# Kernel optimization log

Hardware: AMD Instinct MI355X
Metric: run time of the kernel (lower is better)

The kernel has to match this reference:

```python
import jax, jax.numpy as jnp
import numpy as np

N = 50000      # nodes
E = 800000     # edges (before self loops)
IN = 128       # in_channels
C = 64         # out_channels per head
H = 4          # heads (both layers)
NEG_SLOPE = 0.2


def setup_inputs():
    key = jax.random.key(0)
    ks = jax.random.split(key, 14)
    nrm = lambda k, sh, s: jax.random.normal(k, sh, dtype=jnp.float32) * s
    x = nrm(ks[0], (N, IN), 1.0)
    edge_index = jax.random.randint(ks[1], (2, E), 0, N, dtype=jnp.int32)
    batch = jnp.zeros((N,), dtype=jnp.int32)
    edge_attr = jax.random.uniform(ks[2], (E, 1), dtype=jnp.float32)
    # layer 1 params (PyG GATConv: lin, att_src, att_dst, lin_edge, att_edge, bias)
    W1 = nrm(ks[3], (IN, H * C), 1.0 / np.sqrt(IN))
    We1 = nrm(ks[4], (1, H * C), 1.0)
    att_s1 = nrm(ks[5], (H, C), 1.0 / np.sqrt(C))
    att_d1 = nrm(ks[6], (H, C), 1.0 / np.sqrt(C))
    att_e1 = nrm(ks[7], (H, C), 1.0 / np.sqrt(C))
    b1 = jnp.zeros((H * C,), dtype=jnp.float32)
    # layer 2 params (in = H*C = 256)
    W2 = nrm(ks[8], (H * C, H * C), 1.0 / np.sqrt(H * C))
    We2 = nrm(ks[9], (1, H * C), 1.0)
    att_s2 = nrm(ks[10], (H, C), 1.0 / np.sqrt(C))
    att_d2 = nrm(ks[11], (H, C), 1.0 / np.sqrt(C))
    att_e2 = nrm(ks[12], (H, C), 1.0 / np.sqrt(C))
    b2 = jnp.zeros((H * C,), dtype=jnp.float32)
    return dict(x=x, edge_index=edge_index, batch=batch, edge_attr=edge_attr,
                W1=W1, We1=We1, att_s1=att_s1, att_d1=att_d1, att_e1=att_e1, b1=b1,
                W2=W2, We2=We2, att_s2=att_s2, att_d2=att_d2, att_e2=att_e2, b2=b2)


def gat_layer(h_in, src, dst, e_attr, W, We, att_s, att_d, att_e, b):
    n = h_in.shape[0]
    h = (h_in @ W).reshape(n, H, C)                      # [N,H,C]
    a_src = jnp.einsum('nhc,hc->nh', h, att_s)           # [N,H]
    a_dst = jnp.einsum('nhc,hc->nh', h, att_d)
    e = (e_attr @ We).reshape(-1, H, C)                  # [E',H,C]
    a_edge = jnp.einsum('ehc,hc->eh', e, att_e)          # [E',H]
    alpha = jax.nn.leaky_relu(a_src[src] + a_dst[dst] + a_edge, NEG_SLOPE)
    # softmax over edges grouped by destination node
    amax = jax.ops.segment_max(alpha, dst, num_segments=n)
    amax = jnp.where(jnp.isfinite(amax), amax, 0.0)
    ex = jnp.exp(alpha - amax[dst])
    denom = jax.ops.segment_sum(ex, dst, num_segments=n)
    a = ex / (denom[dst] + 1e-16)                        # [E',H]
    out = jax.ops.segment_sum(a[:, :, None] * h[src], dst, num_segments=n)
    return out.reshape(n, H * C) + b


def reference(x, edge_index, batch, edge_attr,
              W1, We1, att_s1, att_d1, att_e1, b1,
              W2, We2, att_s2, att_d2, att_e2, b2):
    n = x.shape[0]
    # PyG GATConv default: add self loops, self-loop edge_attr = mean fill
    loop = jnp.arange(n, dtype=edge_index.dtype)
    src = jnp.concatenate([edge_index[0], loop])
    dst = jnp.concatenate([edge_index[1], loop])
    ea_fill = jnp.broadcast_to(edge_attr.mean(axis=0, keepdims=True), (n, edge_attr.shape[1]))
    ea = jnp.concatenate([edge_attr, ea_fill], axis=0)
    h1 = gat_layer(x, src, dst, ea, W1, We1, att_s1, att_d1, att_e1, b1)
    h2 = gat_layer(h1, src, dst, ea, W2, We2, att_s2, att_d2, att_e2, b2)
    return h2
```

## Files before the change

### kernel.cpp

```cpp
#include <hip/hip_runtime.h>

#define NEG_SLOPE 0.2f

typedef __attribute__((ext_vector_type(8))) short bf16x8;
typedef __attribute__((ext_vector_type(4))) float f32x4;

__device__ inline unsigned short f2bf(float x) {
  unsigned int u = __float_as_uint(x);
  u += 0x7fffu + ((u >> 16) & 1u);
  return (unsigned short)(u >> 16);
}

__device__ inline unsigned fkey(float x) {
  unsigned u = __float_as_uint(x);
  return (u >> 31) ? ~u : (u | 0x80000000u);
}
__device__ inline float fkey_dec(unsigned k) {
  unsigned u = (k & 0x80000000u) ? (k ^ 0x80000000u) : ~k;
  return __uint_as_float(u);
}


__global__ void hist_mean_kernel(const int* __restrict__ ei, const float* __restrict__ eattr,
                                 int* __restrict__ counts, float* __restrict__ part,
                                 int E, int Etot) {
  int e = blockIdx.x * blockDim.x + threadIdx.x;
  float s = 0.f;
  if (e < Etot) {
    int d = (e < E) ? ei[E + e] : (e - E);
    atomicAdd(&counts[d], 1);
    if (e < E) s = eattr[e];
  }
#pragma unroll
  for (int off = 1; off < 64; off <<= 1) s += __shfl_xor(s, off, 64);
  __shared__ float ws_[4];
  if ((threadIdx.x & 63) == 0) ws_[threadIdx.x >> 6] = s;
  __syncthreads();
  if (threadIdx.x == 0) part[blockIdx.x] = ws_[0] + ws_[1] + ws_[2] + ws_[3];
}

__global__ void scan_blocksum(const int* __restrict__ counts, int* __restrict__ bsum, int Nn) {
  int base = blockIdx.x * 4096 + threadIdx.x * 16;
  int s = 0;
#pragma unroll
  for (int i = 0; i < 16; i++) { int idx = base + i; if (idx < Nn) s += counts[idx]; }
#pragma unroll
  for (int off = 1; off < 64; off <<= 1) s += __shfl_xor(s, off, 64);
  __shared__ int ws_[4];
  if ((threadIdx.x & 63) == 0) ws_[threadIdx.x >> 6] = s;
  __syncthreads();
  if (threadIdx.x == 0) bsum[blockIdx.x] = ws_[0] + ws_[1] + ws_[2] + ws_[3];
}

__global__ void scan_offsets(int* bsum, int nb, int* rowptrN,
                             const float* __restrict__ meanpart, float* meanv,
                             int E, int npart) {
  int t = threadIdx.x;
  float f = 0.f;
  for (int i = t; i < npart; i += 64) f += meanpart[i];
#pragma unroll
  for (int off = 1; off < 64; off <<= 1) f += __shfl_xor(f, off, 64);
  if (t == 0) {
    *meanv = f / (float)E;
    int acc = 0;
    for (int i = 0; i < nb; i++) { int v = bsum[i]; bsum[i] = acc; acc += v; }
    *rowptrN = acc;
  }
}

__global__ void scan_final(const int* __restrict__ counts, const int* __restrict__ bsum,
                           int* __restrict__ rowptr, int* __restrict__ cursor, int Nn) {
  int base = blockIdx.x * 4096 + threadIdx.x * 16;
  int v[16]; int s = 0;
#pragma unroll
  for (int i = 0; i < 16; i++) { int idx = base + i; v[i] = (idx < Nn) ? counts[idx] : 0; s += v[i]; }
  int lane = threadIdx.x & 63, wv = threadIdx.x >> 6;
  int incl = s;
#pragma unroll
  for (int off = 1; off < 64; off <<= 1) {
    int y = __shfl_up(incl, off, 64);
    if (lane >= off) incl += y;
  }
  __shared__ int wtot[4];
  if (lane == 63) wtot[wv] = incl;
  __syncthreads();
  int run = bsum[blockIdx.x] + incl - s;
  for (int i = 0; i < wv; i++) run += wtot[i];
  for (int i = 0; i < 16; i++) {
    int idx = base + i;
    if (idx < Nn) { rowptr[idx] = run; cursor[idx] = run; }
    run += v[i];
  }
}

__global__ void scatter_kernel(const int* __restrict__ ei, const float* __restrict__ eattr,
                               const float* __restrict__ meanv,
                               int* __restrict__ cursor, int2* __restrict__ epack,
                               int E, int Etot) {
  int e = blockIdx.x * blockDim.x + threadIdx.x;
  if (e >= Etot) return;
  int d, s; float ea;
  if (e < E) { d = ei[E + e]; s = ei[e]; ea = eattr[e]; }
  else       { d = e - E;     s = e - E; ea = meanv[0]; }
  int pos = atomicAdd(&cursor[d], 1);
  epack[pos] = make_int2(s, __float_as_int(ea));
}

__global__ void wtrans_kernel(const float* __restrict__ W1, unsigned short* __restrict__ Wt1,
                              const float* __restrict__ W2, unsigned short* __restrict__ Wt2,
                              const float* __restrict__ We1, const float* __restrict__ atte1,
                              const float* __restrict__ We2, const float* __restrict__ atte2,
                              float* __restrict__ weatt1, float* __restrict__ weatt2) {
  int b = blockIdx.x;
  if (b >= 384) {
    int i = threadIdx.x;
#pragma unroll
    for (int l = 0; l < 2; l++) {
      const float* We = l ? We2 : We1;
      const float* at = l ? atte2 : atte1;
      float* wo = l ? weatt2 : weatt1;
      float p = We[i] * at[i];
#pragma unroll
      for (int off = 1; off < 64; off <<= 1) p += __shfl_xor(p, off, 64);
      if ((i & 63) == 0) wo[i >> 6] = p;
    }
    return;
  }
  const float* W; unsigned short* Wt; int K, t;
  if (b < 128) { W = W1; Wt = Wt1; K = 128; t = b * 256 + threadIdx.x; }
  else         { W = W2; Wt = Wt2; K = 256; t = (b - 128) * 256 + threadIdx.x; }
  int n = t & 255, k = t >> 8;
  if (k >= K) return;
  Wt[(size_t)n * K + k] = f2bf(W[(size_t)k * 256 + n]);
}


template <int AF32>
__device__ inline bf16x8 load_a_row(const void* Ain, int gr, int K, int kpos, int M) {
  bf16x8 v = {};
  if (gr < M) {
    if (AF32) {
      const float* src = (const float*)Ain + (size_t)gr * K + kpos;
      float4 f0 = *(const float4*)src;
      float4 f1 = *(const float4*)(src + 4);
      v[0] = (short)f2bf(f0.x); v[1] = (short)f2bf(f0.y);
      v[2] = (short)f2bf(f0.z); v[3] = (short)f2bf(f0.w);
      v[4] = (short)f2bf(f1.x); v[5] = (short)f2bf(f1.y);
      v[6] = (short)f2bf(f1.z); v[7] = (short)f2bf(f1.w);
    } else {
      v = *(const bf16x8*)((const unsigned short*)Ain + (size_t)gr * K + kpos);
    }
  }
  return v;
}

#define CS_STRIDE 264

template <int AF32>
__global__ __launch_bounds__(512) void gemm_att(const void* __restrict__ Ain,
                                                const unsigned short* __restrict__ Wt,
                                                unsigned short* __restrict__ Hb,
                                                const float* __restrict__ atts,
                                                const float* __restrict__ attd,
                                                float* __restrict__ asrc,
                                                float* __restrict__ adst,
                                                unsigned* __restrict__ gmaxk,
                                                int M, int K) {
  __shared__ __align__(16) short smem[(128 + 256) * 64];
  __shared__ float gmx[8];
  short* As = smem;
  short* Bs = smem + 128 * 64;
  short* Cs = smem;
  const int tid = threadIdx.x;
  const int lane = tid & 63, wv = tid >> 6;
  const int wm = wv >> 2, wn = wv & 3;
  const int l15 = lane & 15, l4 = lane >> 4;
  const int bm = blockIdx.x * 128;

  const int r0 = tid >> 3, kc = (tid & 7) * 8;
  const int nbB = tid >> 3, cB = (tid & 7) * 8;

  f32x4 acc[4][4] = {};
  bf16x8 ra0, ra1, rb0, rb1, rb2, rb3;

#define GLOAD_TILE(K0, A0, A1, B0, B1, B2, B3)                                 \
  {                                                                            \
    A0 = load_a_row<AF32>(Ain, bm + r0, K, (K0) + kc, M);                      \
    A1 = load_a_row<AF32>(Ain, bm + r0 + 64, K, (K0) + kc, M);                 \
    B0 = *(const bf16x8*)&Wt[(size_t)(nbB +   0) * K + (K0) + cB];             \
    B1 = *(const bf16x8*)&Wt[(size_t)(nbB +  64) * K + (K0) + cB];             \
    B2 = *(const bf16x8*)&Wt[(size_t)(nbB + 128) * K + (K0) + cB];             \
    B3 = *(const bf16x8*)&Wt[(size_t)(nbB + 192) * K + (K0) + cB];             \
  }

  GLOAD_TILE(0, ra0, ra1, rb0, rb1, rb2, rb3)

  for (int k0 = 0; k0 < K; k0 += 64) {
    *(bf16x8*)&As[((r0) * 64 + kc) ^ ((r0 & 7) << 3)] = ra0;
    *(bf16x8*)&As[((r0 + 64) * 64 + kc) ^ ((r0 & 7) << 3)] = ra1;
    *(bf16x8*)&Bs[((nbB) * 64 + cB) ^ ((nbB & 7) << 3)] = rb0;
    *(bf16x8*)&Bs[((nbB + 64) * 64 + cB) ^ ((nbB & 7) << 3)] = rb1;
    *(bf16x8*)&Bs[((nbB + 128) * 64 + cB) ^ ((nbB & 7) << 3)] = rb2;
    *(bf16x8*)&Bs[((nbB + 192) * 64 + cB) ^ ((nbB & 7) << 3)] = rb3;
    __syncthreads();

    bool more = (k0 + 64 < K);
    bf16x8 na0, na1, nb0, nb1, nb2, nb3;
    if (more) GLOAD_TILE(k0 + 64, na0, na1, nb0, nb1, nb2, nb3)

    bf16x8 af[4][2], bfr[4][2];
#pragma unroll
    for (int rt = 0; rt < 4; rt++)
#pragma unroll
      for (int ks = 0; ks < 2; ks++) {
        int row = wm * 64 + rt * 16 + l15;
        int kb = l4 * 8 + ks * 32;
        af[rt][ks] = *(const bf16x8*)&As[(row * 64 + kb) ^ ((row & 7) << 3)];
      }
#pragma unroll
    for (int ct = 0; ct < 4; ct++)
#pragma unroll
      for (int ks = 0; ks < 2; ks++) {
        int n = wn * 64 + ct * 16 + l15;
        int kb = l4 * 8 + ks * 32;
        bfr[ct][ks] = *(const bf16x8*)&Bs[(n * 64 + kb) ^ ((n & 7) << 3)];
      }
#pragma unroll
    for (int rt = 0; rt < 4; rt++)
#pragma unroll
      for (int ct = 0; ct < 4; ct++)
#pragma unroll
        for (int ks = 0; ks < 2; ks++)
          acc[rt][ct] = __builtin_amdgcn_mfma_f32_16x16x32_bf16(
              af[rt][ks], bfr[ct][ks], acc[rt][ct], 0, 0, 0);
    __syncthreads();

    if (more) { ra0 = na0; ra1 = na1; rb0 = nb0; rb1 = nb1; rb2 = nb2; rb3 = nb3; }
  }
#undef GLOAD_TILE

  float s_att[4], d_att[4];
#pragma unroll
  for (int ct = 0; ct < 4; ct++) {
    s_att[ct] = atts[wn * 64 + ct * 16 + l15];
    d_att[ct] = attd[wn * 64 + ct * 16 + l15];
  }
  float ps[4][4] = {}, pd[4][4] = {};
#pragma unroll
  for (int rt = 0; rt < 4; rt++)
#pragma unroll
    for (int ct = 0; ct < 4; ct++)
#pragma unroll
      for (int i = 0; i < 4; i++) {
        float v = acc[rt][ct][i];
        ps[rt][i] = fmaf(v, s_att[ct], ps[rt][i]);
        pd[rt][i] = fmaf(v, d_att[ct], pd[rt][i]);
      }

#pragma unroll
  for (int rt = 0; rt < 4; rt++)
#pragma unroll
    for (int i = 0; i < 4; i++) {
#pragma unroll
      for (int off = 1; off < 16; off <<= 1) {
        ps[rt][i] += __shfl_xor(ps[rt][i], off, 64);
        pd[rt][i] += __shfl_xor(pd[rt][i], off, 64);
      }
    }
  float mx = ps[0][0];
#pragma unroll
  for (int rt = 0; rt < 4; rt++)
#pragma unroll
    for (int i = 0; i < 4; i++) mx = fmaxf(mx, ps[rt][i]);
  mx = fmaxf(mx, __shfl_xor(mx, 16, 64));
  mx = fmaxf(mx, __shfl_xor(mx, 32, 64));
  if (lane == 0) gmx[wv] = mx;
  if (l15 == 0) {
#pragma unroll
    for (int rt = 0; rt < 4; rt++)
#pragma unroll
      for (int i = 0; i < 4; i++) {
        int gr = bm + wm * 64 + rt * 16 + l4 * 4 + i;
        if (gr < M) {
          asrc[gr * 4 + wn] = ps[rt][i];
          adst[gr * 4 + wn] = pd[rt][i];
        }
      }
  }

  for (int h = 0; h < 2; h++) {
    __syncthreads();
    if (wm == h) {
#pragma unroll
      for (int rt = 0; rt < 4; rt++)
#pragma unroll
        for (int ct = 0; ct < 4; ct++)
#pragma unroll
          for (int i = 0; i < 4; i++) {
            int lrow = rt * 16 + l4 * 4 + i;
            Cs[lrow * CS_STRIDE + wn * 64 + ct * 16 + l15] = f2bf(acc[rt][ct][i]);
          }
    }
    __syncthreads();
    int row = tid >> 3, seg = tid & 7;
    int gr = bm + h * 64 + row;
    if (gr < M) {
      const short* srcr = &Cs[row * CS_STRIDE + seg * 32];
      unsigned short* dstr = &Hb[(size_t)gr * 256 + seg * 32];
#pragma unroll
      for (int k = 0; k < 4; k++)
        *(uint4*)&dstr[k * 8] = *(const uint4*)&srcr[k * 8];
    }
  }

  if (wv < 4 && lane == 0) {
    float m2 = fmaxf(gmx[wv], gmx[wv + 4]);
    atomicMax(&gmaxk[wv * 32], fkey(m2));
  }
}


#define AGG_PH1(CNT)                                                        \
  int src = 0; float w = 0.f;                                               \
  if (il < (CNT)) {                                                         \
    int2 e = epack[p + il];                                                 \
    float al = fmaf(__int_as_float(e.y), wa, asrc[e.x * 4 + hh] + ad);      \
    al = fmaxf(al, NEG_SLOPE * al);                                         \
    w = __expf(al - b);                                                     \
    src = e.x;                                                              \
  }                                                                         \
  ssum += w;

#define AGG_GATHER(i)                                                       \
  {                                                                         \
    int sl = (i) | hb16;                                                    \
    int si = __shfl(src, sl, 64);                                           \
    float wi = __shfl(w, sl, 64);                                           \
    uint2 hv = *(const uint2*)&Hb[(size_t)((unsigned)si * 256u + co)];      \
    acc.x = fmaf(wi, __uint_as_float(hv.x << 16), acc.x);                   \
    acc.y = fmaf(wi, __uint_as_float(hv.x & 0xffff0000u), acc.y);           \
    acc.z = fmaf(wi, __uint_as_float(hv.y << 16), acc.z);                   \
    acc.w = fmaf(wi, __uint_as_float(hv.y & 0xffff0000u), acc.w);           \
  }

template <int OUTBF>
__global__ __launch_bounds__(256) void gat_agg(const unsigned short* __restrict__ Hb,
                                               const float* __restrict__ asrc,
                                               const float* __restrict__ adst,
                                               const int* __restrict__ rowptr,
                                               const int2* __restrict__ epack,
                                               const float* __restrict__ weatt,
                                               const unsigned* __restrict__ gmaxk,
                                               const float* __restrict__ bias,
                                               unsigned short* __restrict__ outb,
                                               float* __restrict__ outf, int Nn) {
  int wid = (blockIdx.x * blockDim.x + threadIdx.x) >> 6;
  int lane = threadIdx.x & 63;
  if (wid >= Nn) return;
  int beg = rowptr[wid], end = rowptr[wid + 1];
  int hh = lane >> 4;
  int il = lane & 15;
  int hb16 = lane & 48;
  float wa = weatt[hh];
  float ad = adst[wid * 4 + hh];
  float braw = ad + fkey_dec(gmaxk[hh * 32]) + fmaxf(wa, 0.f);
  float b = fmaxf(braw, NEG_SLOPE * braw);
  unsigned co = (unsigned)lane * 4u;

  float ssum = 0.f;
  float4 acc = {0.f, 0.f, 0.f, 0.f};

  int p = beg;
  for (; p + 16 <= end; p += 16) {
    AGG_PH1(16)
#pragma unroll
    for (int i = 0; i < 16; i++) AGG_GATHER(i)
  }
  int cnt = end - p;
  if (cnt > 0) {
    AGG_PH1(cnt)
    for (int i = 0; i < cnt; i++) AGG_GATHER(i)
  }

#pragma unroll
  for (int off = 1; off < 16; off <<= 1) ssum += __shfl_xor(ssum, off, 64);

  float inv = 1.f / (ssum + 1e-16f);
  float4 b4 = *(const float4*)&bias[co];
  float4 r;
  r.x = fmaf(acc.x, inv, b4.x);
  r.y = fmaf(acc.y, inv, b4.y);
  r.z = fmaf(acc.z, inv, b4.z);
  r.w = fmaf(acc.w, inv, b4.w);
  if (OUTBF) {
    unsigned lo = (unsigned)f2bf(r.x) | ((unsigned)f2bf(r.y) << 16);
    unsigned hi = (unsigned)f2bf(r.z) | ((unsigned)f2bf(r.w) << 16);
    *(uint2*)&outb[(size_t)wid * 256 + co] = make_uint2(lo, hi);
  } else {
    *(float4*)&outf[(size_t)wid * 256 + co] = r;
  }
}


extern "C" void kernel_launch(void* const* d_in, const int* in_sizes, int n_in,
                              void* d_out, int out_size, void* d_ws, size_t ws_size,
                              hipStream_t stream) {
  (void)n_in; (void)out_size; (void)ws_size;
  const float* x     = (const float*)d_in[0];
  const int*   ei    = (const int*)d_in[1];
  const float* eattr = (const float*)d_in[3];
  const float* W1    = (const float*)d_in[4];
  const float* We1   = (const float*)d_in[5];
  const float* atts1 = (const float*)d_in[6];
  const float* attd1 = (const float*)d_in[7];
  const float* atte1 = (const float*)d_in[8];
  const float* b1    = (const float*)d_in[9];
  const float* W2    = (const float*)d_in[10];
  const float* We2   = (const float*)d_in[11];
  const float* atts2 = (const float*)d_in[12];
  const float* attd2 = (const float*)d_in[13];
  const float* atte2 = (const float*)d_in[14];
  const float* b2    = (const float*)d_in[15];
  float* out = (float*)d_out;

  const int Nn   = in_sizes[0] / 128;
  const int E    = in_sizes[1] / 2;
  const int Etot = E + Nn;
  const int EB   = (Etot + 255) / 256;

  char* p = (char*)d_ws;
  auto alloc = [&](size_t bytes) { void* r = (void*)p; p += (bytes + 255) & ~(size_t)255; return r; };
  int*      counts  = (int*)alloc((size_t)Nn * 4);
  unsigned* gmaxk1  = (unsigned*)alloc(512);
  unsigned* gmaxk2  = (unsigned*)alloc(512);
  char* zero_end = p;
  int*   rowptr  = (int*)alloc((size_t)(Nn + 1) * 4);
  int*   cursor  = (int*)alloc((size_t)Nn * 4);
  int2*  epack   = (int2*)alloc((size_t)Etot * 8);
  int*   bsum    = (int*)alloc(64 * 4);
  float* meanpart= (float*)alloc((size_t)EB * 4);
  float* meanv   = (float*)alloc(4);
  float* weatt1  = (float*)alloc(16);
  float* weatt2  = (float*)alloc(16);
  float* asrc    = (float*)alloc((size_t)Nn * 4 * 4);
  float* adst    = (float*)alloc((size_t)Nn * 4 * 4);
  unsigned short* hbuf = (unsigned short*)alloc((size_t)Nn * 256 * 2);
  unsigned short* h1b  = (unsigned short*)alloc((size_t)Nn * 256 * 2);
  unsigned short* Wt1  = (unsigned short*)alloc((size_t)256 * 128 * 2);
  unsigned short* Wt2  = (unsigned short*)alloc((size_t)256 * 256 * 2);

  const int NB = (Nn + 4095) / 4096;

  hipMemsetAsync(counts, 0, (size_t)(zero_end - (char*)counts), stream);

  hist_mean_kernel<<<EB, 256, 0, stream>>>(ei, eattr, counts, meanpart, E, Etot);
  scan_blocksum<<<NB, 256, 0, stream>>>(counts, bsum, Nn);
  scan_offsets<<<1, 64, 0, stream>>>(bsum, NB, rowptr + Nn, meanpart, meanv, E, EB);
  scan_final<<<NB, 256, 0, stream>>>(counts, bsum, rowptr, cursor, Nn);
  scatter_kernel<<<EB, 256, 0, stream>>>(ei, eattr, meanv, cursor, epack, E, Etot);
  wtrans_kernel<<<385, 256, 0, stream>>>(W1, Wt1, W2, Wt2, We1, atte1, We2, atte2,
                                         weatt1, weatt2);

  const int gemmBlocks = (Nn + 127) / 128;
  const int nodeBlocks = (Nn + 3) / 4;

  gemm_att<1><<<gemmBlocks, 512, 0, stream>>>(x, Wt1, hbuf, atts1, attd1,
                                              asrc, adst, gmaxk1, Nn, 128);
  gat_agg<1><<<nodeBlocks, 256, 0, stream>>>(hbuf, asrc, adst, rowptr, epack,
                                             weatt1, gmaxk1, b1, h1b, nullptr, Nn);
  gemm_att<0><<<gemmBlocks, 512, 0, stream>>>(h1b, Wt2, hbuf, atts2, attd2,
                                              asrc, adst, gmaxk2, Nn, 256);
  gat_agg<0><<<nodeBlocks, 256, 0, stream>>>(hbuf, asrc, adst, rowptr, epack,
                                             weatt2, gmaxk2, b2, nullptr, out, Nn);
}
```

Measured before the change: 328.2 us.

## Split GAT aggregation into 8 column slices with edge-parallel lane groups

The aggregation kernel now launches 8 blocks per group of 4 nodes. Each wavefront handles one 32-column slice of one head for one node, and its 8 lane groups each process different edges in parallel, followed by a cross-group shuffle reduction. This targets the serial per-edge gather latency of the old one-wave-per-node layout, where each edge needed 16 dependent iterations over the full 256-wide row. In exchange, edge metadata and attention weights are recomputed 8 times per node, each gather is only 8 bytes per lane across 8 rows, and the reductions add extra shuffles.

```diff
diff --git a/kernel.cpp b/kernel.cpp
--- a/kernel.cpp
+++ b/kernel.cpp
@@ -320,29 +320,6 @@
 }
 
 
-#define AGG_PH1(CNT)                                                        \
-  int src = 0; float w = 0.f;                                               \
-  if (il < (CNT)) {                                                         \
-    int2 e = epack[p + il];                                                 \
-    float al = fmaf(__int_as_float(e.y), wa, asrc[e.x * 4 + hh] + ad);      \
-    al = fmaxf(al, NEG_SLOPE * al);                                         \
-    w = __expf(al - b);                                                     \
-    src = e.x;                                                              \
-  }                                                                         \
-  ssum += w;
-
-#define AGG_GATHER(i)                                                       \
-  {                                                                         \
-    int sl = (i) | hb16;                                                    \
-    int si = __shfl(src, sl, 64);                                           \
-    float wi = __shfl(w, sl, 64);                                           \
-    uint2 hv = *(const uint2*)&Hb[(size_t)((unsigned)si * 256u + co)];      \
-    acc.x = fmaf(wi, __uint_as_float(hv.x << 16), acc.x);                   \
-    acc.y = fmaf(wi, __uint_as_float(hv.x & 0xffff0000u), acc.y);           \
-    acc.z = fmaf(wi, __uint_as_float(hv.y << 16), acc.z);                   \
-    acc.w = fmaf(wi, __uint_as_float(hv.y & 0xffff0000u), acc.w);           \
-  }
-
 template <int OUTBF>
 __global__ __launch_bounds__(256) void gat_agg(const unsigned short* __restrict__ Hb,
                                                const float* __restrict__ asrc,
@@ -354,50 +331,75 @@
                                                const float* __restrict__ bias,
                                                unsigned short* __restrict__ outb,
                                                float* __restrict__ outf, int Nn) {
-  int wid = (blockIdx.x * blockDim.x + threadIdx.x) >> 6;
-  int lane = threadIdx.x & 63;
+  const int slice = blockIdx.x & 7;
+  const int nb = blockIdx.x >> 3;
+  const int lane = threadIdx.x & 63, wv = threadIdx.x >> 6;
+  const int wid = nb * 4 + wv;
   if (wid >= Nn) return;
-  int beg = rowptr[wid], end = rowptr[wid + 1];
-  int hh = lane >> 4;
-  int il = lane & 15;
-  int hb16 = lane & 48;
+  const int hh = slice >> 1;
+  const int grp = lane >> 3, sub = lane & 7;
+  const unsigned co = (unsigned)(slice * 32 + sub * 4);
   float wa = weatt[hh];
   float ad = adst[wid * 4 + hh];
   float braw = ad + fkey_dec(gmaxk[hh * 32]) + fmaxf(wa, 0.f);
   float b = fmaxf(braw, NEG_SLOPE * braw);
-  unsigned co = (unsigned)lane * 4u;
+  int beg = rowptr[wid], end = rowptr[wid + 1];
 
   float ssum = 0.f;
   float4 acc = {0.f, 0.f, 0.f, 0.f};
 
-  int p = beg;
-  for (; p + 16 <= end; p += 16) {
-    AGG_PH1(16)
-#pragma unroll
-    for (int i = 0; i < 16; i++) AGG_GATHER(i)
-  }
-  int cnt = end - p;
-  if (cnt > 0) {
-    AGG_PH1(cnt)
-    for (int i = 0; i < cnt; i++) AGG_GATHER(i)
-  }
-
-#pragma unroll
-  for (int off = 1; off < 16; off <<= 1) ssum += __shfl_xor(ssum, off, 64);
-
-  float inv = 1.f / (ssum + 1e-16f);
-  float4 b4 = *(const float4*)&bias[co];
-  float4 r;
-  r.x = fmaf(acc.x, inv, b4.x);
-  r.y = fmaf(acc.y, inv, b4.y);
-  r.z = fmaf(acc.z, inv, b4.z);
-  r.w = fmaf(acc.w, inv, b4.w);
-  if (OUTBF) {
-    unsigned lo = (unsigned)f2bf(r.x) | ((unsigned)f2bf(r.y) << 16);
-    unsigned hi = (unsigned)f2bf(r.z) | ((unsigned)f2bf(r.w) << 16);
-    *(uint2*)&outb[(size_t)wid * 256 + co] = make_uint2(lo, hi);
-  } else {
-    *(float4*)&outf[(size_t)wid * 256 + co] = r;
+  for (int p = beg; p < end; p += 64) {
+    int cnt = end - p; if (cnt > 64) cnt = 64;
+    int src = 0; float w = 0.f;
+    if (lane < cnt) {
+      int2 e = epack[p + lane];
+      float al = fmaf(__int_as_float(e.y), wa, asrc[e.x * 4 + hh] + ad);
+      al = fmaxf(al, NEG_SLOPE * al);
+      w = __expf(al - b);
+      src = e.x;
+    }
+    ssum += w;
+    int iters = (cnt + 7) >> 3;
+    for (int it = 0; it < iters; it++) {
+      int j = it * 8 + grp;
+      int jj = (j < cnt) ? j : 0;
+      int si = __shfl(src, jj, 64);
+      float wj = __shfl(w, jj, 64);
+      if (j < cnt) {
+        uint2 hv = *(const uint2*)&Hb[(size_t)((unsigned)si * 256u + co)];
+        acc.x = fmaf(wj, __uint_as_float(hv.x << 16), acc.x);
+        acc.y = fmaf(wj, __uint_as_float(hv.x & 0xffff0000u), acc.y);
+        acc.z = fmaf(wj, __uint_as_float(hv.y << 16), acc.z);
+        acc.w = fmaf(wj, __uint_as_float(hv.y & 0xffff0000u), acc.w);
+      }
+    }
+  }
+
+#pragma unroll
+  for (int off = 8; off < 64; off <<= 1) {
+    acc.x += __shfl_xor(acc.x, off, 64);
+    acc.y += __shfl_xor(acc.y, off, 64);
+    acc.z += __shfl_xor(acc.z, off, 64);
+    acc.w += __shfl_xor(acc.w, off, 64);
+  }
+#pragma unroll
+  for (int off = 1; off < 64; off <<= 1) ssum += __shfl_xor(ssum, off, 64);
+
+  if (grp == 0) {
+    float inv = 1.f / (ssum + 1e-16f);
+    float4 b4 = *(const float4*)&bias[co];
+    float4 r;
+    r.x = fmaf(acc.x, inv, b4.x);
+    r.y = fmaf(acc.y, inv, b4.y);
+    r.z = fmaf(acc.z, inv, b4.z);
+    r.w = fmaf(acc.w, inv, b4.w);
+    if (OUTBF) {
+      unsigned lo = (unsigned)f2bf(r.x) | ((unsigned)f2bf(r.y) << 16);
+      unsigned hi = (unsigned)f2bf(r.z) | ((unsigned)f2bf(r.w) << 16);
+      *(uint2*)&outb[(size_t)wid * 256 + co] = make_uint2(lo, hi);
+    } else {
+      *(float4*)&outf[(size_t)wid * 256 + co] = r;
+    }
   }
 }
 
@@ -462,14 +464,14 @@
                                          weatt1, weatt2);
 
   const int gemmBlocks = (Nn + 127) / 128;
-  const int nodeBlocks = (Nn + 3) / 4;
+  const int aggBlocks  = 8 * ((Nn + 3) / 4);
 
   gemm_att<1><<<gemmBlocks, 512, 0, stream>>>(x, Wt1, hbuf, atts1, attd1,
                                               asrc, adst, gmaxk1, Nn, 128);
-  gat_agg<1><<<nodeBlocks, 256, 0, stream>>>(hbuf, asrc, adst, rowptr, epack,
-                                             weatt1, gmaxk1, b1, h1b, nullptr, Nn);
+  gat_agg<1><<<aggBlocks, 256, 0, stream>>>(hbuf, asrc, adst, rowptr, epack,
+                                            weatt1, gmaxk1, b1, h1b, nullptr, Nn);
   gemm_att<0><<<gemmBlocks, 512, 0, stream>>>(h1b, Wt2, hbuf, atts2, attd2,
                                               asrc, adst, gmaxk2, Nn, 256);
-  gat_agg<0><<<nodeBlocks, 256, 0, stream>>>(hbuf, asrc, adst, rowptr, epack,
-                                             weatt2, gmaxk2, b2, nullptr, out, Nn);
-}
+  gat_agg<0><<<aggBlocks, 256, 0, stream>>>(hbuf, asrc, adst, rowptr, epack,
+                                            weatt2, gmaxk2, b2, nullptr, out, Nn);
+}
```

Result: slower. 545.7 us (+66.3%).
